# Optimization experiments

Measured on AMD Instinct MI355X. Metric: run time of the kernel, lower is better.

The kernel has to match this reference:

```python
import jax, jax.numpy as jnp
import numpy as np

N_NODES = 50000
N_EDGES = 800000
V_IN, V_OUT, E_IN, E_OUT = 128, 64, 64, 64


def setup_inputs() -> dict:
    key = jax.random.key(0)
    ks = jax.random.split(key, 9)
    return {
        "n_feat": jax.random.normal(ks[0], (N_NODES, V_IN), dtype=jnp.float32),
        "e_feat": jax.random.normal(ks[1], (N_EDGES, E_IN), dtype=jnp.float32),
        "src": jax.random.randint(ks[2], (N_EDGES,), 0, N_NODES),
        "dst": jax.random.randint(ks[3], (N_EDGES,), 0, N_NODES),
        "W_a": jax.random.normal(ks[4], (2 * V_IN + E_IN, V_OUT), dtype=jnp.float32) * 0.1,
        "W_T": jax.random.normal(ks[5], (2 * V_IN + E_IN, V_OUT), dtype=jnp.float32) * 0.1,
        "b_T": jnp.zeros((V_OUT,), dtype=jnp.float32),
        "W_e": jax.random.normal(ks[6], (V_IN, E_OUT), dtype=jnp.float32) * 0.1,
        "W_ee": jax.random.normal(ks[7], (E_IN, E_OUT), dtype=jnp.float32) * 0.1,
        "prelu_a": jnp.full((1,), 0.25, dtype=jnp.float32),
    }


def _prelu(x, a):
    return jnp.where(x >= 0, x, a * x)


def reference(n_feat, e_feat, src, dst, W_a, W_T, b_T, W_e, W_ee, prelu_a):
    v, e_in = V_IN, E_IN
    Ns = n_feat[src]            # [E, v_in] gathered source feats
    Nd = n_feat[dst]            # [E, v_in] gathered dest feats
    # concat order in message_function is [N_dst, e, N_src]; split weights instead of
    # materializing the [E, 2v+e] concat.
    Wa_d, Wa_e, Wa_s = W_a[:v], W_a[v:v + e_in], W_a[v + e_in:]
    Wt_d, Wt_e, Wt_s = W_T[:v], W_T[v:v + e_in], W_T[v + e_in:]
    logits = _prelu(Nd @ Wa_d + e_feat @ Wa_e + Ns @ Wa_s, prelu_a)   # [E, v_out]
    unatt = Nd @ Wt_d + e_feat @ Wt_e + Ns @ Wt_s                      # [E, v_out]
    # ragged per-dst-node softmax over incoming-edge mailbox, per feature channel
    m = jax.ops.segment_max(logits, dst, num_segments=N_NODES)         # [N, v_out]
    m = jnp.where(jnp.isfinite(m), m, 0.0)
    ex = jnp.exp(logits - m[dst])                                      # [E, v_out]
    denom = jax.ops.segment_sum(ex, dst, num_segments=N_NODES)         # [N, v_out]
    num = jax.ops.segment_sum(ex * unatt, dst, num_segments=N_NODES)   # [N, v_out]
    deg = jax.ops.segment_sum(jnp.ones((dst.shape[0],), jnp.float32), dst, num_segments=N_NODES)
    has_msg = (deg > 0)[:, None]
    denom_safe = jnp.where(has_msg, denom, 1.0)
    # DGL leaves 0-in-degree nodes at zeros (reduce never called for them)
    new_n_feat = jnp.where(has_msg, num / denom_safe + b_T, 0.0)       # [N, v_out]
    # edge update uses the OLD node features (apply_edges runs before n_feat swap)
    new_e_feat = Ns @ W_e + Nd @ W_e + e_feat @ W_ee                   # [E, e_out]
    return new_n_feat, new_e_feat
```

## Files before the change

kernel.cpp:

```cpp
#include <hip/hip_runtime.h>

#define N_NODES 50000
#define N_EDGES 800000

typedef __attribute__((ext_vector_type(8))) short short8;
typedef __attribute__((ext_vector_type(4))) float f32x4;

__device__ __forceinline__ short bf16_rne(float f) {
  unsigned u = __float_as_uint(f);
  unsigned r = (u + 0x7FFFu + ((u >> 16) & 1u)) >> 16;
  return (short)r;
}

__global__ __launch_bounds__(256) void prep_w(
    const float* __restrict__ W_a, const float* __restrict__ W_T,
    const float* __restrict__ W_e, unsigned short* __restrict__ Wbf) {
  int t = blockIdx.x * 256 + threadIdx.x;
  if (t >= 4 * 20 * 64 * 8) return;
  int kt = t / 10240, rdm = t % 10240;
  int ct = rdm >> 9, L = (rdm >> 3) & 63, j = rdm & 7;
  int k = kt * 32 + (L >> 4) * 8 + j;
  int oc = ct * 16 + (L & 15);
  float v;
  if (oc < 64)       v = W_a[k * 64 + oc];
  else if (oc < 128) v = W_e[k * 64 + (oc - 64)];
  else if (oc < 192) v = W_a[(192 + k) * 64 + (oc - 128)];
  else if (oc < 256) v = W_T[(192 + k) * 64 + (oc - 192)];
  else               v = W_T[k * 64 + (oc - 256)];
  Wbf[t] = (unsigned short)bf16_rne(v);
}

__global__ __launch_bounds__(256) void hist_kernel(
    const int* __restrict__ dst, unsigned* __restrict__ hist) {
  int e = blockIdx.x * 256 + threadIdx.x;
  if (e < N_EDGES) atomicAdd(&hist[dst[e]], 1u);
}

__global__ __launch_bounds__(1024) void scan_cursor(
    const unsigned* __restrict__ hist, unsigned* __restrict__ cursor) {
  __shared__ unsigned sSums[16];
  const int tid = threadIdx.x;
  const int lane = tid & 63;
  const int w = tid >> 6;
  const int CH = (N_NODES + 1023) / 1024;
  const int begin = tid * CH;
  const int end = (begin + CH < N_NODES) ? begin + CH : N_NODES;

  unsigned local = 0;
  for (int i = begin; i < end; ++i) local += hist[i];

  unsigned sum = local;
  #pragma unroll
  for (int off = 1; off < 64; off <<= 1) {
    unsigned t = __shfl_up(sum, off, 64);
    if (lane >= off) sum += t;
  }
  if (lane == 63) sSums[w] = sum;
  __syncthreads();
  if (w == 0) {
    unsigned v = (lane < 16) ? sSums[lane] : 0u;
    unsigned s2 = v;
    #pragma unroll
    for (int off = 1; off < 16; off <<= 1) {
      unsigned t = __shfl_up(s2, off, 64);
      if (lane >= off) s2 += t;
    }
    if (lane < 16) sSums[lane] = s2 - v;
  }
  __syncthreads();

  unsigned run = sSums[w] + (sum - local);
  for (int i = begin; i < end; ++i) {
    cursor[i] = run;
    run += hist[i];
  }
}

__global__ __launch_bounds__(256) void scatter_kernel(
    const int* __restrict__ src, const int* __restrict__ dst,
    unsigned* __restrict__ cursor, int* __restrict__ perm,
    int* __restrict__ ssrc, int* __restrict__ sdst) {
  int e = blockIdx.x * 256 + threadIdx.x;
  if (e >= N_EDGES) return;
  int d = dst[e];
  unsigned pos = atomicAdd(&cursor[d], 1u);
  perm[pos] = e;
  ssrc[pos] = src[e];
  sdst[pos] = d;
}

__global__ __launch_bounds__(256) void node_proj_mfma(
    const float* __restrict__ n_feat, const unsigned short* __restrict__ Wbf,
    uint2* __restrict__ NPs4, float* __restrict__ Ptd) {
  __shared__ short sA[64 * 128];
  const int tid = threadIdx.x;
  const int lane = tid & 63;
  const int wid = tid >> 6;
  const int n0 = blockIdx.x * 64;

  for (int cid = tid; cid < 64 * 16; cid += 256) {
    int nd = cid >> 4, k8 = cid & 15;
    int nsrc = n0 + nd; if (nsrc >= N_NODES) nsrc = N_NODES - 1;
    const float* p = n_feat + (size_t)nsrc * 128 + k8 * 8;
    float4 v0 = *(const float4*)p;
    float4 v1 = *(const float4*)(p + 4);
    short8 a;
    a[0] = bf16_rne(v0.x); a[1] = bf16_rne(v0.y);
    a[2] = bf16_rne(v0.z); a[3] = bf16_rne(v0.w);
    a[4] = bf16_rne(v1.x); a[5] = bf16_rne(v1.y);
    a[6] = bf16_rne(v1.z); a[7] = bf16_rne(v1.w);
    *(short8*)(&sA[nd * 128 + ((k8 ^ (nd & 7)) << 3)]) = a;
  }
  __syncthreads();

  const int row = lane & 15;
  const int q   = lane >> 4;

  short8 afrag[4];
  #pragma unroll
  for (int kt = 0; kt < 4; ++kt) {
    int nd = wid * 16 + row;
    afrag[kt] = *(const short8*)(&sA[nd * 128 + (((kt * 4 + q) ^ (row & 7)) << 3)]);
  }

  const short8* Wb8 = (const short8*)Wbf;
  f32x4 acc[20];
  #pragma unroll
  for (int ct = 0; ct < 20; ++ct) acc[ct] = (f32x4){0.f, 0.f, 0.f, 0.f};
  #pragma unroll
  for (int ct = 0; ct < 20; ++ct)
    #pragma unroll
    for (int kt = 0; kt < 4; ++kt) {
      short8 b = Wb8[(kt * 20 + ct) * 64 + lane];
      acc[ct] = __builtin_amdgcn_mfma_f32_16x16x32_bf16(afrag[kt], b, acc[ct], 0, 0, 0);
    }

  #pragma unroll
  for (int i = 0; i < 4; ++i)
    #pragma unroll
    for (int r = 0; r < 4; ++r) {
      int nd = n0 + wid * 16 + q * 4 + r;
      if (nd < N_NODES) {
        unsigned e16  = (unsigned short)bf16_rne(acc[4  + i][r]);
        unsigned as16 = (unsigned short)bf16_rne(acc[8  + i][r]);
        unsigned ts16 = (unsigned short)bf16_rne(acc[12 + i][r]);
        unsigned ad16 = (unsigned short)bf16_rne(acc[i][r]);
        uint2 v;
        v.x = e16 | (as16 << 16);
        v.y = ts16 | (ad16 << 16);
        NPs4[(size_t)nd * 64 + i * 16 + row] = v;
        Ptd[(size_t)nd * 64 + i * 16 + row] = acc[16 + i][r];
      }
    }
}

__global__ __launch_bounds__(256) void edge_pass_mfma(
    const float* __restrict__ e_feat, const int* __restrict__ perm,
    const int* __restrict__ ssrc, const int* __restrict__ sdst,
    const float* __restrict__ W_a, const float* __restrict__ W_T,
    const float* __restrict__ W_ee, const float* __restrict__ prelu_a,
    const uint2* __restrict__ NPs4,
    float* __restrict__ denom, float* __restrict__ numer,
    float* __restrict__ out_e) {
  __shared__ short sWT[192 * 64];
  __shared__ float sAcc[4][4 * 200];
  const int tid = threadIdx.x;
  const int lane = tid & 63;
  const int wid = tid >> 6;

  for (int idx = tid; idx < 192 * 32; idx += 256) {
    int C = idx >> 5;
    int k = (idx & 31) * 2;
    float f0, f1;
    if (C < 64)       { f0 = W_a[(128 + k) * 64 + C];        f1 = W_a[(129 + k) * 64 + C]; }
    else if (C < 128) { f0 = W_T[(128 + k) * 64 + (C - 64)]; f1 = W_T[(129 + k) * 64 + (C - 64)]; }
    else              { f0 = W_ee[k * 64 + (C - 128)];       f1 = W_ee[(k + 1) * 64 + (C - 128)]; }
    unsigned pack = ((unsigned)(unsigned short)bf16_rne(f0)) |
                    (((unsigned)(unsigned short)bf16_rne(f1)) << 16);
    int sidx = C * 64 + (((k >> 3) ^ (C & 7)) << 3) + (k & 7);
    *(unsigned*)(&sWT[sidx]) = pack;
  }
  __syncthreads();
  const float pa = prelu_a[0];

  const int row = lane & 15;
  const int q   = lane >> 4;
  float* sA = sAcc[wid];

  const int ngroups = N_EDGES / 64;
  for (int g = blockIdx.x; g < ngroups; g += gridDim.x) {
    const int ebase = g * 64 + wid * 16;

    const int sv = ssrc[ebase + row];
    const int dv = sdst[ebase + row];
    const int pv = perm[ebase + row];

    const float* pbase = e_feat + (size_t)pv * 64;
    float4 v00 = *(const float4*)(pbase + q * 8);
    float4 v01 = *(const float4*)(pbase + q * 8 + 4);
    float4 v10 = *(const float4*)(pbase + 32 + q * 8);
    float4 v11 = *(const float4*)(pbase + 32 + q * 8 + 4);

    uint2 ps[16];
    #pragma unroll
    for (int m = 0; m < 16; ++m) {
      int s_m = __builtin_amdgcn_readlane(sv, m);
      ps[m] = NPs4[(size_t)s_m * 64 + lane];
    }

    short8 afrag[2];
    {
      short8 a;
      a[0] = bf16_rne(v00.x); a[1] = bf16_rne(v00.y);
      a[2] = bf16_rne(v00.z); a[3] = bf16_rne(v00.w);
      a[4] = bf16_rne(v01.x); a[5] = bf16_rne(v01.y);
      a[6] = bf16_rne(v01.z); a[7] = bf16_rne(v01.w);
      afrag[0] = a;
      a[0] = bf16_rne(v10.x); a[1] = bf16_rne(v10.y);
      a[2] = bf16_rne(v10.z); a[3] = bf16_rne(v10.w);
      a[4] = bf16_rne(v11.x); a[5] = bf16_rne(v11.y);
      a[6] = bf16_rne(v11.z); a[7] = bf16_rne(v11.w);
      afrag[1] = a;
    }

    f32x4 aa[4], at[4], ae[4];
    #pragma unroll
    for (int ct = 0; ct < 4; ++ct) {
      aa[ct] = (f32x4){0.f, 0.f, 0.f, 0.f};
      at[ct] = (f32x4){0.f, 0.f, 0.f, 0.f};
      ae[ct] = (f32x4){0.f, 0.f, 0.f, 0.f};
    }
    #pragma unroll
    for (int kt = 0; kt < 2; ++kt)
      #pragma unroll
      for (int ct = 0; ct < 4; ++ct) {
        int c = ct * 16 + row;
        int kg = ((kt * 4 + q) ^ (c & 7)) << 3;
        short8 ba = *(const short8*)(&sWT[(c)       * 64 + kg]);
        short8 bt = *(const short8*)(&sWT[(64 + c)  * 64 + kg]);
        short8 be = *(const short8*)(&sWT[(128 + c) * 64 + kg]);
        aa[ct] = __builtin_amdgcn_mfma_f32_16x16x32_bf16(afrag[kt], ba, aa[ct], 0, 0, 0);
        at[ct] = __builtin_amdgcn_mfma_f32_16x16x32_bf16(afrag[kt], bt, at[ct], 0, 0, 0);
        ae[ct] = __builtin_amdgcn_mfma_f32_16x16x32_bf16(afrag[kt], be, ae[ct], 0, 0, 0);
      }

    int dA = -1, dB = -1;
    float dsA = 0.f, nsA = 0.f, eA = 0.f, adA = 0.f;
    float dsB = 0.f, nsB = 0.f, eB = 0.f, adB = 0.f;

    #pragma unroll
    for (int r = 0; r < 4; ++r) {
      #pragma unroll
      for (int ct = 0; ct < 4; ++ct) {
        sA[q * 200 +       ct * 16 + row] = aa[ct][r];
        sA[q * 200 +  64 + ct * 16 + row] = at[ct][r];
        sA[q * 200 + 128 + ct * 16 + row] = ae[ct][r];
      }
      #pragma unroll
      for (int j = 0; j < 4; ++j) {
        const int m = j * 4 + r;
        int d  = __builtin_amdgcn_readlane(dv, m);
        int eo = __builtin_amdgcn_readlane(pv, m);
        float e_s  = __uint_as_float(ps[m].x << 16);
        float as_s = __uint_as_float(ps[m].x & 0xFFFF0000u);
        float ts_s = __uint_as_float(ps[m].y << 16);
        float aaE = sA[j * 200 + lane];
        float atE = sA[j * 200 + 64 + lane];
        float aeE = sA[j * 200 + 128 + lane];

        float e_d, ad_d;
        bool inA;
        if (d == dA) { e_d = eA; ad_d = adA; inA = true; }
        else if (d == dB) { e_d = eB; ad_d = adB; inA = false; }
        else {
          uint2 pdv = NPs4[(size_t)d * 64 + lane];
          e_d  = __uint_as_float(pdv.x << 16);
          ad_d = __uint_as_float(pdv.y & 0xFFFF0000u);
          if (dA < 0) { dA = d; dsA = 0.f; nsA = 0.f; eA = e_d; adA = ad_d; inA = true; }
          else {
            if (dB >= 0) {
              atomicAdd(denom + (size_t)dB * 64 + lane, dsB);
              atomicAdd(numer + (size_t)dB * 64 + lane, nsB);
            }
            dB = d; dsB = 0.f; nsB = 0.f; eB = e_d; adB = ad_d; inA = false;
          }
        }

        float la = ad_d + aaE + as_s;
        float lg = la >= 0.f ? la : pa * la;
        float ex = __expf(lg);
        float exun = ex * (atE + ts_s);
        out_e[(size_t)eo * 64 + lane] = e_s + e_d + aeE;

        if (inA) { dsA += ex; nsA += exun; }
        else     { dsB += ex; nsB += exun; }
      }
    }
    if (dA >= 0) {
      atomicAdd(denom + (size_t)dA * 64 + lane, dsA);
      atomicAdd(numer + (size_t)dA * 64 + lane, nsA);
    }
    if (dB >= 0) {
      atomicAdd(denom + (size_t)dB * 64 + lane, dsB);
      atomicAdd(numer + (size_t)dB * 64 + lane, nsB);
    }
  }
}

__global__ __launch_bounds__(256) void node_final(
    const float* __restrict__ denom, const float* __restrict__ numer,
    const float* __restrict__ Ptd, const float* __restrict__ b_T,
    float* __restrict__ out_n) {
  int t = blockIdx.x * 256 + threadIdx.x;
  if (t >= N_NODES * 64) return;
  float dn = denom[t];
  out_n[t] = dn > 0.f ? numer[t] / dn + Ptd[t] + b_T[t & 63] : 0.f;
}

extern "C" void kernel_launch(void* const* d_in, const int* in_sizes, int n_in,
                              void* d_out, int out_size, void* d_ws, size_t ws_size,
                              hipStream_t stream) {
  const float* n_feat  = (const float*)d_in[0];
  const float* e_feat  = (const float*)d_in[1];
  const int*   src     = (const int*)d_in[2];
  const int*   dst     = (const int*)d_in[3];
  const float* W_a     = (const float*)d_in[4];
  const float* W_T     = (const float*)d_in[5];
  const float* b_T     = (const float*)d_in[6];
  const float* W_e     = (const float*)d_in[7];
  const float* W_ee    = (const float*)d_in[8];
  const float* prelu_a = (const float*)d_in[9];

  float* out_n = (float*)d_out;
  float* out_e = out_n + (size_t)N_NODES * 64;

  uint2* NPs4  = (uint2*)d_ws;
  float* Ptd   = (float*)((char*)d_ws + (size_t)N_NODES * 64 * 8);
  float* denom = Ptd + (size_t)N_NODES * 64;
  float* numer = denom + (size_t)N_NODES * 64;
  unsigned short* Wbf = (unsigned short*)(numer + (size_t)N_NODES * 64);
  unsigned* hist   = (unsigned*)(Wbf + 40960);
  unsigned* cursor = hist + N_NODES;
  int* perm = (int*)(cursor + N_NODES);
  int* ssrc = perm + N_EDGES;
  int* sdst = ssrc + N_EDGES;

  hipMemsetAsync(denom, 0, (size_t)N_NODES * 64 * 2 * sizeof(float), stream);
  hipMemsetAsync(hist, 0, (size_t)N_NODES * sizeof(unsigned), stream);

  prep_w<<<160, 256, 0, stream>>>(W_a, W_T, W_e, Wbf);
  hist_kernel<<<(N_EDGES + 255) / 256, 256, 0, stream>>>(dst, hist);
  scan_cursor<<<1, 1024, 0, stream>>>(hist, cursor);
  scatter_kernel<<<(N_EDGES + 255) / 256, 256, 0, stream>>>(src, dst, cursor,
                                                            perm, ssrc, sdst);
  node_proj_mfma<<<(N_NODES + 63) / 64, 256, 0, stream>>>(n_feat, Wbf, NPs4, Ptd);
  edge_pass_mfma<<<2048, 256, 0, stream>>>(e_feat, perm, ssrc, sdst, W_a, W_T,
                                           W_ee, prelu_a, NPs4, denom, numer, out_e);
  node_final<<<(N_NODES * 64 + 255) / 256, 256, 0, stream>>>(denom, numer, Ptd, b_T, out_n);
}
```

Before: 424.4 us.

## Merge hist and weight prep kernels, pack src/perm, widen edge blocks to 512

```diff
diff --git a/kernel.cpp b/kernel.cpp
--- a/kernel.cpp
+++ b/kernel.cpp
@@ -12,28 +12,29 @@
   return (short)r;
 }
 
-__global__ __launch_bounds__(256) void prep_w(
+__global__ __launch_bounds__(256) void hist_prep(
+    const int* __restrict__ dst, unsigned* __restrict__ hist,
     const float* __restrict__ W_a, const float* __restrict__ W_T,
     const float* __restrict__ W_e, unsigned short* __restrict__ Wbf) {
-  int t = blockIdx.x * 256 + threadIdx.x;
-  if (t >= 4 * 20 * 64 * 8) return;
-  int kt = t / 10240, rdm = t % 10240;
-  int ct = rdm >> 9, L = (rdm >> 3) & 63, j = rdm & 7;
-  int k = kt * 32 + (L >> 4) * 8 + j;
-  int oc = ct * 16 + (L & 15);
-  float v;
-  if (oc < 64)       v = W_a[k * 64 + oc];
-  else if (oc < 128) v = W_e[k * 64 + (oc - 64)];
-  else if (oc < 192) v = W_a[(192 + k) * 64 + (oc - 128)];
-  else if (oc < 256) v = W_T[(192 + k) * 64 + (oc - 192)];
-  else               v = W_T[k * 64 + (oc - 256)];
-  Wbf[t] = (unsigned short)bf16_rne(v);
-}
-
-__global__ __launch_bounds__(256) void hist_kernel(
-    const int* __restrict__ dst, unsigned* __restrict__ hist) {
-  int e = blockIdx.x * 256 + threadIdx.x;
-  if (e < N_EDGES) atomicAdd(&hist[dst[e]], 1u);
+  const int bid = blockIdx.x;
+  if (bid < N_EDGES / 256) {
+    int e = bid * 256 + threadIdx.x;
+    atomicAdd(&hist[dst[e]], 1u);
+  } else {
+    int t = (bid - N_EDGES / 256) * 256 + threadIdx.x;
+    if (t >= 4 * 20 * 64 * 8) return;
+    int kt = t / 10240, rdm = t % 10240;
+    int ct = rdm >> 9, L = (rdm >> 3) & 63, j = rdm & 7;
+    int k = kt * 32 + (L >> 4) * 8 + j;
+    int oc = ct * 16 + (L & 15);
+    float v;
+    if (oc < 64)       v = W_a[k * 64 + oc];
+    else if (oc < 128) v = W_e[k * 64 + (oc - 64)];
+    else if (oc < 192) v = W_a[(192 + k) * 64 + (oc - 128)];
+    else if (oc < 256) v = W_T[(192 + k) * 64 + (oc - 192)];
+    else               v = W_T[k * 64 + (oc - 256)];
+    Wbf[t] = (unsigned short)bf16_rne(v);
+  }
 }
 
 __global__ __launch_bounds__(1024) void scan_cursor(
@@ -78,14 +79,13 @@
 
 __global__ __launch_bounds__(256) void scatter_kernel(
     const int* __restrict__ src, const int* __restrict__ dst,
-    unsigned* __restrict__ cursor, int* __restrict__ perm,
-    int* __restrict__ ssrc, int* __restrict__ sdst) {
+    unsigned* __restrict__ cursor, int2* __restrict__ se,
+    int* __restrict__ sdst) {
   int e = blockIdx.x * 256 + threadIdx.x;
   if (e >= N_EDGES) return;
   int d = dst[e];
   unsigned pos = atomicAdd(&cursor[d], 1u);
-  perm[pos] = e;
-  ssrc[pos] = src[e];
+  se[pos] = make_int2(src[e], e);
   sdst[pos] = d;
 }
 
@@ -154,21 +154,21 @@
     }
 }
 
-__global__ __launch_bounds__(256) void edge_pass_mfma(
-    const float* __restrict__ e_feat, const int* __restrict__ perm,
-    const int* __restrict__ ssrc, const int* __restrict__ sdst,
+__global__ __launch_bounds__(512, 6) void edge_pass_mfma(
+    const float* __restrict__ e_feat, const int2* __restrict__ se,
+    const int* __restrict__ sdst,
     const float* __restrict__ W_a, const float* __restrict__ W_T,
     const float* __restrict__ W_ee, const float* __restrict__ prelu_a,
     const uint2* __restrict__ NPs4,
     float* __restrict__ denom, float* __restrict__ numer,
     float* __restrict__ out_e) {
   __shared__ short sWT[192 * 64];
-  __shared__ float sAcc[4][4 * 200];
+  __shared__ float sAcc[8][4 * 200];
   const int tid = threadIdx.x;
   const int lane = tid & 63;
   const int wid = tid >> 6;
 
-  for (int idx = tid; idx < 192 * 32; idx += 256) {
+  for (int idx = tid; idx < 192 * 32; idx += 512) {
     int C = idx >> 5;
     int k = (idx & 31) * 2;
     float f0, f1;
@@ -187,13 +187,14 @@
   const int q   = lane >> 4;
   float* sA = sAcc[wid];
 
-  const int ngroups = N_EDGES / 64;
+  const int ngroups = N_EDGES / 128;
   for (int g = blockIdx.x; g < ngroups; g += gridDim.x) {
-    const int ebase = g * 64 + wid * 16;
-
-    const int sv = ssrc[ebase + row];
+    const int ebase = g * 128 + wid * 16;
+
+    const int2 se2 = se[ebase + row];
     const int dv = sdst[ebase + row];
-    const int pv = perm[ebase + row];
+    const int sv = se2.x;
+    const int pv = se2.y;
 
     const float* pbase = e_feat + (size_t)pv * 64;
     float4 v00 = *(const float4*)(pbase + q * 8);
@@ -341,20 +342,17 @@
   unsigned short* Wbf = (unsigned short*)(numer + (size_t)N_NODES * 64);
   unsigned* hist   = (unsigned*)(Wbf + 40960);
   unsigned* cursor = hist + N_NODES;
-  int* perm = (int*)(cursor + N_NODES);
-  int* ssrc = perm + N_EDGES;
-  int* sdst = ssrc + N_EDGES;
+  int2* se = (int2*)(cursor + N_NODES);
+  int* sdst = (int*)(se + N_EDGES);
 
   hipMemsetAsync(denom, 0, (size_t)N_NODES * 64 * 2 * sizeof(float), stream);
   hipMemsetAsync(hist, 0, (size_t)N_NODES * sizeof(unsigned), stream);
 
-  prep_w<<<160, 256, 0, stream>>>(W_a, W_T, W_e, Wbf);
-  hist_kernel<<<(N_EDGES + 255) / 256, 256, 0, stream>>>(dst, hist);
+  hist_prep<<<N_EDGES / 256 + 160, 256, 0, stream>>>(dst, hist, W_a, W_T, W_e, Wbf);
   scan_cursor<<<1, 1024, 0, stream>>>(hist, cursor);
-  scatter_kernel<<<(N_EDGES + 255) / 256, 256, 0, stream>>>(src, dst, cursor,
-                                                            perm, ssrc, sdst);
+  scatter_kernel<<<(N_EDGES + 255) / 256, 256, 0, stream>>>(src, dst, cursor, se, sdst);
   node_proj_mfma<<<(N_NODES + 63) / 64, 256, 0, stream>>>(n_feat, Wbf, NPs4, Ptd);
-  edge_pass_mfma<<<2048, 256, 0, stream>>>(e_feat, perm, ssrc, sdst, W_a, W_T,
-                                           W_ee, prelu_a, NPs4, denom, numer, out_e);
+  edge_pass_mfma<<<2048, 512, 0, stream>>>(e_feat, se, sdst, W_a, W_T, W_ee,
+                                           prelu_a, NPs4, denom, numer, out_e);
   node_final<<<(N_NODES * 64 + 255) / 256, 256, 0, stream>>>(denom, numer, Ptd, b_T, out_n);
 }
```

Result: slower. 816.6 us (+92.4%).
